# Kernel tuning notes

Hardware: AMD Instinct MI355X
Metric: run time of the kernel (lower is better)

The kernel has to match this reference:

```python
import jax, jax.numpy as jnp
import numpy as np

B, S, D, H = 1, 4096, 1024, 16
HD = D // H  # head_dim = 64
NEG = -1e9

def setup_inputs() -> dict:
    key = jax.random.key(0)
    ks = jax.random.split(key, 5)
    scale = 1.0 / np.sqrt(D)
    x = jax.random.normal(ks[0], (B, S, D), dtype=jnp.float32)
    Wq = jax.random.normal(ks[1], (D, D), dtype=jnp.float32) * scale
    Wk = jax.random.normal(ks[2], (D, D), dtype=jnp.float32) * scale
    Wv = jax.random.normal(ks[3], (D, D), dtype=jnp.float32) * scale
    Wo = jax.random.normal(ks[4], (D, D), dtype=jnp.float32) * scale
    mask = jnp.tril(jnp.ones((S, S), dtype=bool))[None, None]  # [1,1,S,S] causal
    return {"x": x, "mask": mask, "Wq": Wq, "Wk": Wk, "Wv": Wv, "Wo": Wo}

def reference(x, mask, Wq, Wk, Wv, Wo):
    # Linear projections (bias=False). nn.Linear computes x @ W.T; weights here
    # are stored as [out, in] so we use x @ W.T for faithfulness.
    q = x @ Wq.T  # [B,S,D]
    k = x @ Wk.T
    v = x @ Wv.T
    def split_heads(t):
        return t.reshape(B, S, H, HD).transpose(0, 2, 1, 3)  # [B,H,S,HD]
    q, k, v = split_heads(q), split_heads(k), split_heads(v)
    scores = jnp.einsum("bhqd,bhkd->bhqk", q, k) / jnp.sqrt(jnp.float32(HD))
    scores = jnp.where(mask, scores, NEG)
    attn = jax.nn.softmax(scores, axis=-1)  # dropout p=0.0 -> identity
    out = jnp.einsum("bhqk,bhkd->bhqd", attn, v)  # [B,H,S,HD]
    out = out.transpose(0, 2, 1, 3).reshape(B, S, D)
    return out @ Wo.T
```

## Files before the change

### kernel.cpp

```cpp
#include <hip/hip_runtime.h>
#include <hip/hip_bf16.h>


typedef __bf16 bf16x8 __attribute__((ext_vector_type(8)));
typedef __bf16 bf16x4 __attribute__((ext_vector_type(4)));
typedef float f32x4 __attribute__((ext_vector_type(4)));
typedef short s16x4 __attribute__((ext_vector_type(4)));

#define GAS __attribute__((address_space(1)))
#define LAS __attribute__((address_space(3)))

__device__ __forceinline__ void async_copy16(const void* g, void* l) {
  __builtin_amdgcn_global_load_lds((const GAS unsigned int*)g,
                                   (LAS unsigned int*)l, 16, 0, 0);
}

__device__ __forceinline__ f32x4 mfma_k16(bf16x4 a, bf16x4 b, f32x4 c) {
  union { bf16x4 h; s16x4 s; } ua, ub;
  ua.h = a; ub.h = b;
  return __builtin_amdgcn_mfma_f32_16x16x16bf16_1k(ua.s, ub.s, c, 0, 0, 0);
}

__global__ __launch_bounds__(256) void cvt_all(const float* __restrict__ x,
                                               const float* __restrict__ Wq,
                                               const float* __restrict__ Wk,
                                               const float* __restrict__ Wv,
                                               const float* __restrict__ Wo,
                                               __bf16* __restrict__ xb,
                                               __bf16* __restrict__ Wc,
                                               __bf16* __restrict__ Wob) {
  int b = blockIdx.x;
  const float* src;
  __bf16* dst;
  if (b < 4096)      { src = x  + (b       ) * 1024; dst = xb  + (long)b * 1024; }
  else if (b < 5120) { src = Wq + (b - 4096) * 1024; dst = Wc  + (long)(b - 4096) * 1024; }
  else if (b < 6144) { src = Wk + (b - 5120) * 1024; dst = Wc  + (1l << 20) + (long)(b - 5120) * 1024; }
  else if (b < 7168) { src = Wv + (b - 6144) * 1024; dst = Wc  + (2l << 20) + (long)(b - 6144) * 1024; }
  else               { src = Wo + (b - 7168) * 1024; dst = Wob + (long)(b - 7168) * 1024; }
  int i = threadIdx.x * 4;
  float4 f = *(const float4*)(src + i);
  bf16x4 o;
  o[0] = (__bf16)f.x; o[1] = (__bf16)f.y; o[2] = (__bf16)f.z; o[3] = (__bf16)f.w;
  *(bf16x4*)(dst + i) = o;
}

__global__ __launch_bounds__(256) void gemm_qkv(const __bf16* __restrict__ A,
                                                const __bf16* __restrict__ B,
                                                __bf16* __restrict__ Qb,
                                                __bf16* __restrict__ Kf,
                                                __bf16* __restrict__ Vf) {
  const int K = 1024;
  __shared__ __bf16 As[128 * 32];
  __shared__ __bf16 Bs[128 * 32];
  const int tid = threadIdx.x;
  const int lane = tid & 63, wv = tid >> 6;
  const int l15 = lane & 15, quad = lane >> 4;
  const int wm = wv >> 1, wn = wv & 1;
  const int bb = blockIdx.x;
  const int xcd = bb & 7, q = bb >> 3;
  const int nb = xcd * 3 + (q % 3);
  const int mb = q / 3;
  const int mbase = mb * 128, nbase = nb * 128;
  const bool swp = (nbase < 2048);

  f32x4 acc[4][4] = {};

  for (int k0 = 0; k0 < K; k0 += 32) {
    __syncthreads();
#pragma unroll
    for (int p = 0; p < 2; ++p) {
      int i = p * 256 + tid;
      int row = i >> 2, kg = i & 3;
      const __bf16* ga = A + (long)(mbase + row) * K + k0 + kg * 8;
      const __bf16* gb = B + (long)(nbase + row) * K + k0 + kg * 8;
      char* la = (char*)As + (p * 256 + wv * 64) * 16;
      char* lb = (char*)Bs + (p * 256 + wv * 64) * 16;
      async_copy16(ga, la);
      async_copy16(gb, lb);
    }
    __syncthreads();
    bf16x8 af[4], bfr[4];
#pragma unroll
    for (int i = 0; i < 4; ++i)
      af[i] = *(const bf16x8*)&As[(wm * 64 + i * 16 + l15) * 32 + quad * 8];
#pragma unroll
    for (int j = 0; j < 4; ++j)
      bfr[j] = *(const bf16x8*)&Bs[(wn * 64 + j * 16 + l15) * 32 + quad * 8];
    if (swp) {
#pragma unroll
      for (int i = 0; i < 4; ++i)
#pragma unroll
        for (int j = 0; j < 4; ++j)
          acc[i][j] = __builtin_amdgcn_mfma_f32_16x16x32_bf16(bfr[j], af[i], acc[i][j], 0, 0, 0);
    } else {
#pragma unroll
      for (int i = 0; i < 4; ++i)
#pragma unroll
        for (int j = 0; j < 4; ++j)
          acc[i][j] = __builtin_amdgcn_mfma_f32_16x16x32_bf16(af[i], bfr[j], acc[i][j], 0, 0, 0);
    }
  }

  if (nbase < 1024) {
    const float QS = 0.18033688011112043f;
#pragma unroll
    for (int i = 0; i < 4; ++i) {
      int row = mbase + wm * 64 + i * 16 + l15;
#pragma unroll
      for (int j = 0; j < 4; ++j) {
        int cb = nbase + wn * 64 + j * 16 + quad * 4;
        union { __bf16 b[4]; uint2 u; } pk;
#pragma unroll
        for (int r = 0; r < 4; ++r) pk.b[r] = (__bf16)(acc[i][j][r] * QS);
        *(uint2*)(Qb + (long)row * 1024 + cb) = pk.u;
      }
    }
  } else if (nbase < 2048) {
#pragma unroll
    for (int i = 0; i < 4; ++i)
#pragma unroll
      for (int j = 0; j < 4; ++j) {
        int d0 = nbase - 1024 + wn * 64 + j * 16 + quad * 4;
        int h = d0 >> 6, dd = d0 & 63;
        int kk = dd >> 5, qf = (dd >> 3) & 3, e0 = dd & 7;
        int kt = mbase + wm * 64 + i * 16 + l15;
        int tile = kt >> 6;
        long off = ((long)(h * 64 + tile) * 8 + i * 2 + kk) * 512 + (qf * 16 + l15) * 8 + e0;
        union { __bf16 b[4]; uint2 u; } pk;
#pragma unroll
        for (int r = 0; r < 4; ++r) pk.b[r] = (__bf16)acc[i][j][r];
        *(uint2*)(Kf + off) = pk.u;
      }
  } else {
#pragma unroll
    for (int i = 0; i < 4; ++i)
#pragma unroll
      for (int j = 0; j < 4; ++j) {
        int col = nbase - 2048 + wn * 64 + j * 16 + l15;
        int h = col >> 6, dd = col & 63;
        int jd = dd >> 4, lv = dd & 15;
        int kt0 = mbase + wm * 64 + i * 16 + quad * 4;
        int tile = kt0 >> 6, w6 = kt0 & 63;
        int jp = w6 >> 5, bit4 = (w6 >> 4) & 1, qv = (w6 >> 2) & 3;
        long off = ((long)(h * 64 + tile) * 8 + jd * 2 + jp) * 512 + (qv * 16 + lv) * 8 + bit4 * 4;
        union { __bf16 b[4]; uint2 u; } pk;
#pragma unroll
        for (int r = 0; r < 4; ++r) pk.b[r] = (__bf16)acc[i][j][r];
        *(uint2*)(Vf + off) = pk.u;
      }
  }
}

__global__ __launch_bounds__(256) void gemm_wo(const __bf16* __restrict__ A,
                                               const __bf16* __restrict__ B,
                                               float* __restrict__ C) {
  const int K = 1024, N = 1024;
  __shared__ __bf16 As[128 * 32];
  __shared__ __bf16 Bs[64 * 32];
  const int tid = threadIdx.x;
  const int lane = tid & 63, wv = tid >> 6;
  const int l15 = lane & 15, quad = lane >> 4;
  const int wm = wv >> 1, wn = wv & 1;
  const int bb = blockIdx.x;
  const int xcd = bb & 7, q = bb >> 3;
  const int nb = xcd * 2 + (q & 1);
  const int mb = q >> 1;
  const int mbase = mb * 128, nbase = nb * 64;

  f32x4 acc[4][2] = {};

  for (int k0 = 0; k0 < K; k0 += 32) {
    __syncthreads();
#pragma unroll
    for (int p = 0; p < 2; ++p) {
      int i = p * 256 + tid;
      int row = i >> 2, kg = i & 3;
      const __bf16* ga = A + (long)(mbase + row) * K + k0 + kg * 8;
      char* la = (char*)As + (p * 256 + wv * 64) * 16;
      async_copy16(ga, la);
    }
    {
      int row = tid >> 2, kg = tid & 3;
      const __bf16* gb = B + (long)(nbase + row) * K + k0 + kg * 8;
      char* lb = (char*)Bs + (wv * 64) * 16;
      async_copy16(gb, lb);
    }
    __syncthreads();
    bf16x8 af[4], bfr[2];
#pragma unroll
    for (int i = 0; i < 4; ++i)
      af[i] = *(const bf16x8*)&As[(wm * 64 + i * 16 + l15) * 32 + quad * 8];
#pragma unroll
    for (int j = 0; j < 2; ++j)
      bfr[j] = *(const bf16x8*)&Bs[(wn * 32 + j * 16 + l15) * 32 + quad * 8];
#pragma unroll
    for (int i = 0; i < 4; ++i)
#pragma unroll
      for (int j = 0; j < 2; ++j)
        acc[i][j] = __builtin_amdgcn_mfma_f32_16x16x32_bf16(bfr[j], af[i], acc[i][j], 0, 0, 0);
  }
#pragma unroll
  for (int i = 0; i < 4; ++i) {
    int row = mbase + wm * 64 + i * 16 + l15;
#pragma unroll
    for (int j = 0; j < 2; ++j) {
      int cb = nbase + wn * 32 + j * 16 + quad * 4;
      *(f32x4*)(C + (long)row * N + cb) = acc[i][j];
    }
  }
}

__global__ __launch_bounds__(512, 2) void flash_attn(const __bf16* __restrict__ Qb,
                                                     const __bf16* __restrict__ Kf,
                                                     const __bf16* __restrict__ Vf,
                                                     __bf16* __restrict__ AO) {
  __shared__ float Ms[4][64][35];
  const int tid = threadIdx.x;
  const int lane = tid & 63, l15 = lane & 15, quad = lane >> 4;
  const int w = tid >> 6;
  const int pr = w >> 1, half = w & 1;
  const int b = blockIdx.x;
  const int h = (b & 7) + 8 * ((b >> 3) & 1);
  const int rest = b >> 4;
  const int P = rest * 4 + pr;
  const int hoff = h * 64;

  const __bf16* Kh = Kf + (long)h * 64 * 4096;
  const __bf16* Vh = Vf + (long)h * 64 * 4096;

  for (int pass = 0; pass < 2; ++pass) {
    const int T = pass ? (127 - P) : P;
    bf16x8 qf[2][2];
#pragma unroll
    for (int g = 0; g < 2; ++g) {
      const int qrow = T * 32 + g * 16 + l15;
      qf[g][0] = *(const bf16x8*)(Qb + (long)qrow * 1024 + hoff + quad * 8);
      qf[g][1] = *(const bf16x8*)(Qb + (long)qrow * 1024 + hoff + 32 + quad * 8);
    }

    const int nkt = (T >> 1) + 1;
    const int kt0 = half ? (nkt >> 1) : 0;
    const int kt1 = half ? nkt : (nkt >> 1);
    f32x4 o_acc[2][4] = {};
    float l_acc[2] = {0.0f, 0.0f};

    bf16x8 kc[8];
    if (kt0 < kt1) {
      const __bf16* Kt = Kh + (long)kt0 * 4096;
#pragma unroll
      for (int f = 0; f < 8; ++f)
        kc[f] = *(const bf16x8*)(Kt + f * 512 + lane * 8);
    }

    for (int kt = kt0; kt < kt1; ++kt) {
      const __bf16* Vt = Vh + (long)kt * 4096;

      bf16x8 va[8];
#pragma unroll
      for (int f = 0; f < 8; ++f)
        va[f] = *(const bf16x8*)(Vt + f * 512 + lane * 8);

      f32x4 st[2][4] = {};
#pragma unroll
      for (int g = 0; g < 2; ++g)
#pragma unroll
        for (int j = 0; j < 4; ++j) {
          st[g][j] = __builtin_amdgcn_mfma_f32_16x16x32_bf16(kc[j * 2 + 0], qf[g][0], st[g][j], 0, 0, 0);
          st[g][j] = __builtin_amdgcn_mfma_f32_16x16x32_bf16(kc[j * 2 + 1], qf[g][1], st[g][j], 0, 0, 0);
        }

      if (kt + 1 < kt1) {
        const __bf16* Kt = Kh + (long)(kt + 1) * 4096;
#pragma unroll
        for (int f = 0; f < 8; ++f)
          kc[f] = *(const bf16x8*)(Kt + f * 512 + lane * 8);
      }

      if (kt == nkt - 1) {
#pragma unroll
        for (int g = 0; g < 2; ++g) {
          const int dq = (T & 1) * 32 + g * 16 + l15;
#pragma unroll
          for (int j = 0; j < 4; ++j)
#pragma unroll
            for (int r = 0; r < 4; ++r)
              if (j * 16 + quad * 4 + r > dq) st[g][j][r] = -3.0e38f;
        }
      }

      bf16x4 pb[2][4];
#pragma unroll
      for (int g = 0; g < 2; ++g) {
        float ps = 0.0f;
#pragma unroll
        for (int j = 0; j < 4; ++j) {
          f32x4 pj;
#pragma unroll
          for (int r = 0; r < 4; ++r) pj[r] = __builtin_amdgcn_exp2f(st[g][j][r]);
          ps += (pj[0] + pj[1]) + (pj[2] + pj[3]);
          bf16x4 bb16;
#pragma unroll
          for (int r = 0; r < 4; ++r) bb16[r] = (__bf16)pj[r];
          pb[g][j] = bb16;
        }
        l_acc[g] += ps;
      }

#pragma unroll
      for (int g = 0; g < 2; ++g)
#pragma unroll
        for (int j = 0; j < 4; ++j) {
          bf16x4 pbj = pb[g][j];
#pragma unroll
          for (int jd = 0; jd < 4; ++jd) {
            bf16x8 v8 = va[jd * 2 + (j >> 1)];
            bf16x4 a4 = (j & 1) ? __builtin_shufflevector(v8, v8, 4, 5, 6, 7)
                                : __builtin_shufflevector(v8, v8, 0, 1, 2, 3);
            o_acc[g][jd] = mfma_k16(a4, pbj, o_acc[g][jd]);
          }
        }
    }

    if (half) {
#pragma unroll
      for (int g = 0; g < 2; ++g) {
#pragma unroll
        for (int jd = 0; jd < 4; ++jd)
#pragma unroll
          for (int r = 0; r < 4; ++r)
            Ms[pr][lane][g * 16 + jd * 4 + r] = o_acc[g][jd][r];
        Ms[pr][lane][32 + g] = l_acc[g];
      }
    }
    __syncthreads();
    if (!half) {
#pragma unroll
      for (int g = 0; g < 2; ++g) {
#pragma unroll
        for (int jd = 0; jd < 4; ++jd)
#pragma unroll
          for (int r = 0; r < 4; ++r)
            o_acc[g][jd][r] += Ms[pr][lane][g * 16 + jd * 4 + r];
        float la = l_acc[g] + Ms[pr][lane][32 + g];
        la += __shfl_xor(la, 16);
        la += __shfl_xor(la, 32);
        const float inv = 1.0f / la;
        const int qrow = T * 32 + g * 16 + l15;
#pragma unroll
        for (int jd = 0; jd < 4; ++jd) {
          bf16x4 ob;
#pragma unroll
          for (int r = 0; r < 4; ++r) ob[r] = (__bf16)(o_acc[g][jd][r] * inv);
          *(bf16x4*)(AO + (long)qrow * 1024 + hoff + jd * 16 + quad * 4) = ob;
        }
      }
    }
    __syncthreads();
  }
}

extern "C" void kernel_launch(void* const* d_in, const int* in_sizes, int n_in,
                              void* d_out, int out_size, void* d_ws, size_t ws_size,
                              hipStream_t stream) {
  const float* x  = (const float*)d_in[0];
  const float* Wq = (const float*)d_in[2];
  const float* Wk = (const float*)d_in[3];
  const float* Wv = (const float*)d_in[4];
  const float* Wo = (const float*)d_in[5];
  float* out = (float*)d_out;

  char* ws = (char*)d_ws;
  __bf16* xb  = (__bf16*)ws;
  __bf16* Wc  = (__bf16*)(ws + (8u << 20));
  __bf16* Wob = (__bf16*)(ws + (14u << 20));
  __bf16* Qb  = (__bf16*)(ws + (16u << 20));
  __bf16* Kfr = (__bf16*)(ws + (24u << 20));
  __bf16* Vfr = (__bf16*)(ws + (32u << 20));
  __bf16* AO  = (__bf16*)(ws + (40u << 20));

  cvt_all<<<8192, 256, 0, stream>>>(x, Wq, Wk, Wv, Wo, xb, Wc, Wob);

  gemm_qkv<<<768, 256, 0, stream>>>(xb, Wc, Qb, Kfr, Vfr);

  flash_attn<<<256, 512, 0, stream>>>(Qb, Kfr, Vfr, AO);

  gemm_wo<<<512, 256, 0, stream>>>(AO, Wob, out);
}
```

Before: 232.8 us.

## Use 64-row query tiles per wave in flash attention, halving K/V reloads

Each wave now processes 64 query rows (four 16-row groups) against each loaded K/V tile, where before it handled 32 rows over two passes. The block shrinks to 256 threads: two wave pairs take a short and a long causal tile (P and 63-P) to balance work, and the grid doubles to 512 blocks. This amortizes each K/V global load over twice as many query rows and removes the per-pass loop and its extra syncs. In exchange it raises register pressure (larger o_acc and qf arrays, now 4x4 accumulators) and gives coarser per-wave load balance.

```diff
diff --git a/kernel.cpp b/kernel.cpp
--- a/kernel.cpp
+++ b/kernel.cpp
@@ -210,66 +210,64 @@
   }
 }
 
-__global__ __launch_bounds__(512, 2) void flash_attn(const __bf16* __restrict__ Qb,
+__global__ __launch_bounds__(256, 2) void flash_attn(const __bf16* __restrict__ Qb,
                                                      const __bf16* __restrict__ Kf,
                                                      const __bf16* __restrict__ Vf,
                                                      __bf16* __restrict__ AO) {
-  __shared__ float Ms[4][64][35];
+  __shared__ float Ms[2][64][69];
   const int tid = threadIdx.x;
   const int lane = tid & 63, l15 = lane & 15, quad = lane >> 4;
   const int w = tid >> 6;
-  const int pr = w >> 1, half = w & 1;
+  const int pairw = w >> 1, half = w & 1;
   const int b = blockIdx.x;
   const int h = (b & 7) + 8 * ((b >> 3) & 1);
-  const int rest = b >> 4;
-  const int P = rest * 4 + pr;
+  const int P = b >> 4;
+  const int T = pairw ? P : (63 - P);
   const int hoff = h * 64;
 
   const __bf16* Kh = Kf + (long)h * 64 * 4096;
   const __bf16* Vh = Vf + (long)h * 64 * 4096;
 
-  for (int pass = 0; pass < 2; ++pass) {
-    const int T = pass ? (127 - P) : P;
-    bf16x8 qf[2][2];
-#pragma unroll
-    for (int g = 0; g < 2; ++g) {
-      const int qrow = T * 32 + g * 16 + l15;
-      qf[g][0] = *(const bf16x8*)(Qb + (long)qrow * 1024 + hoff + quad * 8);
-      qf[g][1] = *(const bf16x8*)(Qb + (long)qrow * 1024 + hoff + 32 + quad * 8);
-    }
-
-    const int nkt = (T >> 1) + 1;
-    const int kt0 = half ? (nkt >> 1) : 0;
-    const int kt1 = half ? nkt : (nkt >> 1);
-    f32x4 o_acc[2][4] = {};
-    float l_acc[2] = {0.0f, 0.0f};
-
-    bf16x8 kc[8];
-    if (kt0 < kt1) {
-      const __bf16* Kt = Kh + (long)kt0 * 4096;
-#pragma unroll
-      for (int f = 0; f < 8; ++f)
-        kc[f] = *(const bf16x8*)(Kt + f * 512 + lane * 8);
-    }
-
-    for (int kt = kt0; kt < kt1; ++kt) {
-      const __bf16* Vt = Vh + (long)kt * 4096;
-
-      bf16x8 va[8];
-#pragma unroll
-      for (int f = 0; f < 8; ++f)
-        va[f] = *(const bf16x8*)(Vt + f * 512 + lane * 8);
-
-      f32x4 st[2][4] = {};
-#pragma unroll
-      for (int g = 0; g < 2; ++g)
-#pragma unroll
-        for (int j = 0; j < 4; ++j) {
-          st[g][j] = __builtin_amdgcn_mfma_f32_16x16x32_bf16(kc[j * 2 + 0], qf[g][0], st[g][j], 0, 0, 0);
-          st[g][j] = __builtin_amdgcn_mfma_f32_16x16x32_bf16(kc[j * 2 + 1], qf[g][1], st[g][j], 0, 0, 0);
-        }
-
-      if (kt + 1 < kt1) {
+  bf16x8 qf[4][2];
+#pragma unroll
+  for (int g = 0; g < 4; ++g) {
+    const int qrow = T * 64 + g * 16 + l15;
+    qf[g][0] = *(const bf16x8*)(Qb + (long)qrow * 1024 + hoff + quad * 8);
+    qf[g][1] = *(const bf16x8*)(Qb + (long)qrow * 1024 + hoff + 32 + quad * 8);
+  }
+
+  const int nkt = T + 1;
+  const int kt0 = half ? (nkt >> 1) : 0;
+  const int kt1 = half ? nkt : (nkt >> 1);
+  f32x4 o_acc[4][4] = {};
+  float l_acc[4] = {0.0f, 0.0f, 0.0f, 0.0f};
+
+  bf16x8 kc[8];
+  if (kt0 < kt1) {
+    const __bf16* Kt = Kh + (long)kt0 * 4096;
+#pragma unroll
+    for (int f = 0; f < 8; ++f)
+      kc[f] = *(const bf16x8*)(Kt + f * 512 + lane * 8);
+  }
+
+  for (int kt = kt0; kt < kt1; ++kt) {
+    const __bf16* Vt = Vh + (long)kt * 4096;
+
+    bf16x8 va[8];
+#pragma unroll
+    for (int f = 0; f < 8; ++f)
+      va[f] = *(const bf16x8*)(Vt + f * 512 + lane * 8);
+
+#pragma unroll
+    for (int g = 0; g < 4; ++g) {
+      f32x4 st[4] = {};
+#pragma unroll
+      for (int j = 0; j < 4; ++j) {
+        st[j] = __builtin_amdgcn_mfma_f32_16x16x32_bf16(kc[j * 2 + 0], qf[g][0], st[j], 0, 0, 0);
+        st[j] = __builtin_amdgcn_mfma_f32_16x16x32_bf16(kc[j * 2 + 1], qf[g][1], st[j], 0, 0, 0);
+      }
+
+      if (g == 3 && kt + 1 < kt1) {
         const __bf16* Kt = Kh + (long)(kt + 1) * 4096;
 #pragma unroll
         for (int f = 0; f < 8; ++f)
@@ -277,85 +275,76 @@
       }
 
       if (kt == nkt - 1) {
-#pragma unroll
-        for (int g = 0; g < 2; ++g) {
-          const int dq = (T & 1) * 32 + g * 16 + l15;
-#pragma unroll
-          for (int j = 0; j < 4; ++j)
-#pragma unroll
-            for (int r = 0; r < 4; ++r)
-              if (j * 16 + quad * 4 + r > dq) st[g][j][r] = -3.0e38f;
+        const int dq = g * 16 + l15;
+#pragma unroll
+        for (int j = 0; j < 4; ++j)
+#pragma unroll
+          for (int r = 0; r < 4; ++r)
+            if (j * 16 + quad * 4 + r > dq) st[j][r] = -3.0e38f;
+      }
+
+      bf16x4 pb[4];
+      float ps = 0.0f;
+#pragma unroll
+      for (int j = 0; j < 4; ++j) {
+        f32x4 pj;
+#pragma unroll
+        for (int r = 0; r < 4; ++r) pj[r] = __builtin_amdgcn_exp2f(st[j][r]);
+        ps += (pj[0] + pj[1]) + (pj[2] + pj[3]);
+        bf16x4 bb16;
+#pragma unroll
+        for (int r = 0; r < 4; ++r) bb16[r] = (__bf16)pj[r];
+        pb[j] = bb16;
+      }
+      l_acc[g] += ps;
+
+#pragma unroll
+      for (int j = 0; j < 4; ++j) {
+        bf16x4 pbj = pb[j];
+#pragma unroll
+        for (int jd = 0; jd < 4; ++jd) {
+          bf16x8 v8 = va[jd * 2 + (j >> 1)];
+          bf16x4 a4 = (j & 1) ? __builtin_shufflevector(v8, v8, 4, 5, 6, 7)
+                              : __builtin_shufflevector(v8, v8, 0, 1, 2, 3);
+          o_acc[g][jd] = mfma_k16(a4, pbj, o_acc[g][jd]);
         }
       }
-
-      bf16x4 pb[2][4];
-#pragma unroll
-      for (int g = 0; g < 2; ++g) {
-        float ps = 0.0f;
-#pragma unroll
-        for (int j = 0; j < 4; ++j) {
-          f32x4 pj;
-#pragma unroll
-          for (int r = 0; r < 4; ++r) pj[r] = __builtin_amdgcn_exp2f(st[g][j][r]);
-          ps += (pj[0] + pj[1]) + (pj[2] + pj[3]);
-          bf16x4 bb16;
-#pragma unroll
-          for (int r = 0; r < 4; ++r) bb16[r] = (__bf16)pj[r];
-          pb[g][j] = bb16;
-        }
-        l_acc[g] += ps;
-      }
-
-#pragma unroll
-      for (int g = 0; g < 2; ++g)
-#pragma unroll
-        for (int j = 0; j < 4; ++j) {
-          bf16x4 pbj = pb[g][j];
-#pragma unroll
-          for (int jd = 0; jd < 4; ++jd) {
-            bf16x8 v8 = va[jd * 2 + (j >> 1)];
-            bf16x4 a4 = (j & 1) ? __builtin_shufflevector(v8, v8, 4, 5, 6, 7)
-                                : __builtin_shufflevector(v8, v8, 0, 1, 2, 3);
-            o_acc[g][jd] = mfma_k16(a4, pbj, o_acc[g][jd]);
-          }
-        }
-    }
-
-    if (half) {
-#pragma unroll
-      for (int g = 0; g < 2; ++g) {
-#pragma unroll
-        for (int jd = 0; jd < 4; ++jd)
-#pragma unroll
-          for (int r = 0; r < 4; ++r)
-            Ms[pr][lane][g * 16 + jd * 4 + r] = o_acc[g][jd][r];
-        Ms[pr][lane][32 + g] = l_acc[g];
-      }
-    }
-    __syncthreads();
-    if (!half) {
-#pragma unroll
-      for (int g = 0; g < 2; ++g) {
-#pragma unroll
-        for (int jd = 0; jd < 4; ++jd)
-#pragma unroll
-          for (int r = 0; r < 4; ++r)
-            o_acc[g][jd][r] += Ms[pr][lane][g * 16 + jd * 4 + r];
-        float la = l_acc[g] + Ms[pr][lane][32 + g];
-        la += __shfl_xor(la, 16);
-        la += __shfl_xor(la, 32);
-        const float inv = 1.0f / la;
-        const int qrow = T * 32 + g * 16 + l15;
-#pragma unroll
-        for (int jd = 0; jd < 4; ++jd) {
-          bf16x4 ob;
-#pragma unroll
-          for (int r = 0; r < 4; ++r) ob[r] = (__bf16)(o_acc[g][jd][r] * inv);
-          *(bf16x4*)(AO + (long)qrow * 1024 + hoff + jd * 16 + quad * 4) = ob;
-        }
-      }
-    }
-    __syncthreads();
+    }
+  }
+
+  if (half) {
+#pragma unroll
+    for (int g = 0; g < 4; ++g) {
+#pragma unroll
+      for (int jd = 0; jd < 4; ++jd)
+#pragma unroll
+        for (int r = 0; r < 4; ++r)
+          Ms[pairw][lane][g * 16 + jd * 4 + r] = o_acc[g][jd][r];
+      Ms[pairw][lane][64 + g] = l_acc[g];
+    }
+  }
+  __syncthreads();
+  if (!half) {
+#pragma unroll
+    for (int g = 0; g < 4; ++g) {
+#pragma unroll
+      for (int jd = 0; jd < 4; ++jd)
+#pragma unroll
+        for (int r = 0; r < 4; ++r)
+          o_acc[g][jd][r] += Ms[pairw][lane][g * 16 + jd * 4 + r];
+      float la = l_acc[g] + Ms[pairw][lane][64 + g];
+      la += __shfl_xor(la, 16);
+      la += __shfl_xor(la, 32);
+      const float inv = 1.0f / la;
+      const int qrow = T * 64 + g * 16 + l15;
+#pragma unroll
+      for (int jd = 0; jd < 4; ++jd) {
+        bf16x4 ob;
+#pragma unroll
+        for (int r = 0; r < 4; ++r) ob[r] = (__bf16)(o_acc[g][jd][r] * inv);
+        *(bf16x4*)(AO + (long)qrow * 1024 + hoff + jd * 16 + quad * 4) = ob;
+      }
+    }
   }
 }
 
@@ -382,7 +371,7 @@
 
   gemm_qkv<<<768, 256, 0, stream>>>(xb, Wc, Qb, Kfr, Vfr);
 
-  flash_attn<<<256, 512, 0, stream>>>(Qb, Kfr, Vfr, AO);
+  flash_attn<<<512, 256, 0, stream>>>(Qb, Kfr, Vfr, AO);
 
   gemm_wo<<<512, 256, 0, stream>>>(AO, Wob, out);
 }
```

After: 250.8 us. 1.08x slower.
